# Optimization experiments

Measured on AMD Instinct MI355X. Metric: run time of the kernel, lower is better.

## Reference

```python
import jax, jax.numpy as jnp
import numpy as np

NEG_SLOPE = 0.2  # PyG GATConv default leaky_relu slope
BN_EPS = 1e-5


def gat_conv(x_src, x_dst, src, dst, w_src, w_dst, att_src, att_dst, bias):
    """Bipartite PyG GATConv, heads=H, concat=False (mean over heads), add_self_loops=True.
    x_src: [Ns, F], x_dst: [Nd, F]; src/dst: [E] int edge index; w_*: [F, H*C]; att_*: [H, C]; bias: [C].
    """
    H, C = att_src.shape
    n_dst = x_dst.shape[0]
    hs = (x_src @ w_src).reshape(-1, H, C)            # [Ns, H, C]
    hd = (x_dst @ w_dst).reshape(-1, H, C)            # [Nd, H, C]
    a_s = (hs * att_src[None]).sum(-1)                # [Ns, H]
    a_d = (hd * att_dst[None]).sum(-1)                # [Nd, H]
    # PyG adds self loops with num_nodes = min(Ns, Nd) for bipartite inputs
    n_loop = min(x_src.shape[0], n_dst)
    loop = jnp.arange(n_loop, dtype=src.dtype)
    src = jnp.concatenate([src, loop])
    dst = jnp.concatenate([dst, loop])
    e = jax.nn.leaky_relu(a_s[src] + a_d[dst], NEG_SLOPE)           # [E+L, H]
    m = jax.ops.segment_max(e, dst, num_segments=n_dst)             # [Nd, H]
    ex = jnp.exp(e - m[dst])
    den = jax.ops.segment_sum(ex, dst, num_segments=n_dst)
    alpha = ex / (den[dst] + 1e-16)                                 # neighborhood softmax
    msg = hs[src] * alpha[:, :, None]                               # [E+L, H, C]
    out = jax.ops.segment_sum(msg, dst, num_segments=n_dst)         # [Nd, H, C]
    return out.mean(axis=1) + bias


def _forward(user_ids, ingredient_ids, recipe_x, ing_src, ing_dst, ub_src, ub_dst,
             user_table, ing_table, W_rl, b_rl, bn_gamma, bn_beta,
             g1_ws, g1_wd, g1_as, g1_ad, g1_b,
             g2_ws, g2_wd, g2_as, g2_ad, g2_b):
    # nn.Embedding(max_norm=1.0): renorm looked-up rows to L2 norm <= 1
    u = user_table[user_ids]
    un = jnp.linalg.norm(u, axis=-1, keepdims=True)
    u = u * jnp.where(un > 1.0, 1.0 / (un + 1e-7), 1.0)
    # static ingredient embedding lookup
    ing = ing_table[ingredient_ids]
    # recipe linear + BatchNorm (training-mode batch stats; dropout off = eval)
    r = recipe_x @ W_rl + b_rl
    mu = r.mean(axis=0)
    var = ((r - mu) ** 2).mean(axis=0)
    r = bn_gamma * (r - mu) * jax.lax.rsqrt(var + BN_EPS) + bn_beta
    # ingredient -> recipe GAT, residual add
    r = r + gat_conv(ing, r, ing_src, ing_dst, g1_ws, g1_wd, g1_as, g1_ad, g1_b)
    # user -> recipe GAT
    r = gat_conv(u, r, ub_src, ub_dst, g2_ws, g2_wd, g2_as, g2_ad, g2_b)
    return r


def setup_inputs() -> dict:
    key = jax.random.key(0)
    ks = jax.random.split(key, 24)
    NU, NR, NI = 50000, 100000, 20000
    D_IN, H, C = 20, 2, 128
    E1, E2 = 400000, 800000
    s = 0.05
    f32 = jnp.float32
    inp = {
        "user_ids": jax.random.randint(ks[0], (NU,), 0, NU, dtype=jnp.int32),
        "ingredient_ids": jax.random.randint(ks[1], (NI,), 0, NI, dtype=jnp.int32),
        "recipe_x": jax.random.normal(ks[2], (NR, D_IN), f32),
        "ing_src": jax.random.randint(ks[3], (E1,), 0, NI, dtype=jnp.int32),
        "ing_dst": jax.random.randint(ks[4], (E1,), 0, NR, dtype=jnp.int32),
        "ub_src": jax.random.randint(ks[5], (E2,), 0, NU, dtype=jnp.int32),
        "ub_dst": jax.random.randint(ks[6], (E2,), 0, NR, dtype=jnp.int32),
        "user_table": jax.random.normal(ks[7], (NU, C), f32) * s,
        "ing_table": jax.random.normal(ks[8], (NI, C), f32) * s,
        "W_rl": jax.random.normal(ks[9], (D_IN, C), f32) * s,
        "b_rl": jnp.zeros((C,), f32),
        "bn_gamma": jnp.ones((C,), f32),
        "bn_beta": jnp.zeros((C,), f32),
        "g1_ws": jax.random.normal(ks[10], (C, H * C), f32) * s,
        "g1_wd": jax.random.normal(ks[11], (C, H * C), f32) * s,
        "g1_as": jax.random.normal(ks[12], (H, C), f32) * s,
        "g1_ad": jax.random.normal(ks[13], (H, C), f32) * s,
        "g1_b": jnp.zeros((C,), f32),
        "g2_ws": jax.random.normal(ks[14], (C, H * C), f32) * s,
        "g2_wd": jax.random.normal(ks[15], (C, H * C), f32) * s,
        "g2_as": jax.random.normal(ks[16], (H, C), f32) * s,
        "g2_ad": jax.random.normal(ks[17], (H, C), f32) * s,
        "g2_b": jnp.zeros((C,), f32),
    }
    return inp


def reference(user_ids, ingredient_ids, recipe_x, ing_src, ing_dst, ub_src, ub_dst,
              user_table, ing_table, W_rl, b_rl, bn_gamma, bn_beta,
              g1_ws, g1_wd, g1_as, g1_ad, g1_b,
              g2_ws, g2_wd, g2_as, g2_ad, g2_b):
    return _forward(user_ids, ingredient_ids, recipe_x, ing_src, ing_dst, ub_src, ub_dst,
                    user_table, ing_table, W_rl, b_rl, bn_gamma, bn_beta,
                    g1_ws, g1_wd, g1_as, g1_ad, g1_b,
                    g2_ws, g2_wd, g2_as, g2_ad, g2_b)
```

## Files before the change

### kernel.cpp

```cpp
#include <hip/hip_runtime.h>
#include <hip/hip_bf16.h>
#include <math.h>

#define DIN 20
#define C 128
#define HC 256
#define EB2 2048
#define MAXNB 400
#define CAP 8192
#define CAPSH 13

typedef unsigned short u16;
typedef unsigned int u32;
typedef unsigned long long u64;
typedef __bf16 bf16x8 __attribute__((ext_vector_type(8)));
typedef float f32x4 __attribute__((ext_vector_type(4)));

__device__ __forceinline__ float bfbits2f(unsigned int lo16) {
    return __uint_as_float(lo16 << 16);
}
__device__ __forceinline__ u16 f2bf_rne(float f) {
    unsigned int b = __float_as_uint(f);
    return (u16)((b + 0x7FFFu + ((b >> 16) & 1u)) >> 16);
}

__device__ __forceinline__ void scan512f(u32* cnt, u32* off, u32* wsum4) {
    int t = threadIdx.x;
    int l = t & 63, w = t >> 6;
    u32 a = cnt[2 * t], b = cnt[2 * t + 1];
    u32 s = a + b;
    u32 isc = s;
    #pragma unroll
    for (int o = 1; o < 64; o <<= 1) {
        u32 n = __shfl_up(isc, o);
        if (l >= o) isc += n;
    }
    if (l == 63) wsum4[w] = isc;
    __syncthreads();
    u32 pre = 0;
    if (w > 0) pre += wsum4[0];
    if (w > 1) pre += wsum4[1];
    if (w > 2) pre += wsum4[2];
    u32 excl = pre + isc - s;
    off[2 * t] = excl;
    off[2 * t + 1] = excl + a;
    __syncthreads();
}

__device__ __forceinline__ void edge_at(int i, const int* s1, const int* d1,
    const int* s2, const int* d2, int E1, int T1, int E2, int NR,
    int& s, int& key)
{
    if (i < T1) {
        if (i < E1) { s = s1[i]; key = d1[i]; }
        else        { s = i - E1; key = i - E1; }
    } else {
        int k = i - T1;
        if (k < E2) { s = s2[k]; key = NR + d2[k]; }
        else        { s = k - E2; key = NR + (k - E2); }
    }
}

__global__ __launch_bounds__(256) void k_init(const float* __restrict__ x, int NR,
    float* __restrict__ stats, int SB, int A2B,
    const int* __restrict__ src1, const int* __restrict__ dst1,
    const int* __restrict__ src2, const int* __restrict__ dst2,
    int E1, int L1, int E2, int L2, int NB,
    u32* __restrict__ bucketFill, u64* __restrict__ pairs,
    const float* __restrict__ g2_ws, u16* __restrict__ wsp,
    const float* __restrict__ g1_wd, const float* __restrict__ g1_ad,
    const float* __restrict__ g2_wd, const float* __restrict__ g2_ad,
    const float* __restrict__ g1_ws, const float* __restrict__ g1_as,
    const float* __restrict__ g2_as)
{
    __shared__ __align__(16) char sm[40528];
    int t = threadIdx.x;
    int bid = blockIdx.x;
    if (bid < SB) {
        float (*L)[DIN] = (float(*)[DIN])sm;
        int r = bid * 256 + t;
        if (r < NR) {
            const float4* xp = (const float4*)(x + (size_t)r * DIN);
            float4 v0 = xp[0], v1 = xp[1], v2 = xp[2], v3 = xp[3], v4 = xp[4];
            L[t][0] = v0.x; L[t][1] = v0.y; L[t][2] = v0.z; L[t][3] = v0.w;
            L[t][4] = v1.x; L[t][5] = v1.y; L[t][6] = v1.z; L[t][7] = v1.w;
            L[t][8] = v2.x; L[t][9] = v2.y; L[t][10] = v2.z; L[t][11] = v2.w;
            L[t][12] = v3.x; L[t][13] = v3.y; L[t][14] = v3.z; L[t][15] = v3.w;
            L[t][16] = v4.x; L[t][17] = v4.y; L[t][18] = v4.z; L[t][19] = v4.w;
        } else {
            #pragma unroll
            for (int k = 0; k < DIN; k++) L[t][k] = 0.f;
        }
        __syncthreads();
        if (t < 210) {
            int p = 0, q = t;
            while (q >= DIN - p) { q -= (DIN - p); p++; }
            q += p;
            float acc = 0.f;
            for (int rr = 0; rr < 256; rr++) acc += L[rr][p] * L[rr][q];
            atomicAdd(&stats[p * DIN + q], acc);
            if (p != q) atomicAdd(&stats[q * DIN + p], acc);
        } else if (t < 230) {
            int k = t - 210;
            float acc = 0.f;
            for (int rr = 0; rr < 256; rr++) acc += L[rr][k];
            atomicAdd(&stats[400 + k], acc);
        }
        return;
    }
    if (bid < SB + A2B) {
        u64* ldsE = (u64*)sm;
        u64* ldsS = ldsE + EB2;
        u32* cntA = (u32*)(ldsS + EB2);
        u32* cntB = cntA + 512;
        u32* offL = cntB + 512;
        u32* wsum4 = offL + 512;
        u32* gbase = wsum4 + 4;
        for (int i = t; i < 512; i += 256) { cntA[i] = 0; cntB[i] = 0; }
        __syncthreads();
        int T1 = E1 + L1, T = T1 + E2 + L2;
        int base = (bid - SB) * EB2;
        int nE = T - base; if (nE > EB2) nE = EB2;
        for (int j = t; j < nE; j += 256) {
            int s, key;
            edge_at(base + j, src1, dst1, src2, dst2, E1, T1, E2, NR, s, key);
            ldsE[j] = ((u64)(u32)key << 32) | (u32)s;
            atomicAdd(&cntA[key >> 9], 1u);
        }
        __syncthreads();
        scan512f(cntA, offL, wsum4);
        for (int b = t; b < NB; b += 256) {
            u32 c = cntA[b];
            gbase[b] = c ? (((u32)b << CAPSH) + atomicAdd(&bucketFill[b], c)) : 0u;
        }
        __syncthreads();
        for (int j = t; j < nE; j += 256) {
            u64 e = ldsE[j];
            u32 b = ((u32)(e >> 32)) >> 9;
            u32 r = atomicAdd(&cntB[b], 1u);
            ldsS[offL[b] + r] = e;
        }
        __syncthreads();
        for (int j = t; j < nE; j += 256) {
            u64 e = ldsS[j];
            u32 b = ((u32)(e >> 32)) >> 9;
            pairs[gbase[b] + ((u32)j - offL[b])] = e;
        }
        return;
    }
    if (bid < SB + A2B + 32) {
        int idx0 = ((bid - SB - A2B) * 256 + t) * 4;
        #pragma unroll
        for (int i = 0; i < 4; i++) {
            int flat = idx0 + i;
            int j = flat & 7;
            int lane = (flat >> 3) & 63;
            int kb = (flat >> 9) & 3;
            int nt = flat >> 11;
            int k = kb * 32 + (lane >> 4) * 8 + j;
            int n = nt * 16 + (lane & 15);
            wsp[flat] = f2bf_rne(g2_ws[k * HC + n]);
        }
        return;
    }
    int dr = bid - SB - A2B - 32;
    const float* wm = (dr == 0) ? g1_wd : (dr == 1) ? g2_wd : (dr == 2) ? g1_ws : g2_ws;
    const float* am = (dr == 0) ? g1_ad : (dr == 1) ? g2_ad : (dr == 2) ? g1_as : g2_as;
    int obase = (dr == 0) ? 676 : (dr == 1) ? 932 : (dr == 2) ? 1200 : 1456;
    {
        int k = t >> 1, h = t & 1;
        const float4* wp = (const float4*)(wm + k * HC + h * C);
        const float4* ap = (const float4*)(am + h * C);
        float acc = 0.f;
        #pragma unroll 4
        for (int q = 0; q < 32; q++) {
            float4 xv = wp[q], yv = ap[q];
            acc += xv.x * yv.x + xv.y * yv.y + xv.z * yv.z + xv.w * yv.w;
        }
        stats[obase + t] = acc;
    }
}

__global__ __launch_bounds__(256) void k_pre(float* __restrict__ stats,
    const float* __restrict__ W,
    const float* __restrict__ gamma, const float* __restrict__ beta,
    const float* __restrict__ g1_ws, const float* __restrict__ g1b, float invN)
{
    int t = threadIdx.x;
    __shared__ float Sm[420];
    __shared__ float Wm[DIN * C];
    __shared__ float vd1s[256];
    __shared__ float vd2s[256];
    __shared__ float sS[128];
    __shared__ float sSh[128];
    for (int i = t; i < 420; i += 256) Sm[i] = stats[i];
    for (int i = t; i < DIN * C; i += 256) Wm[i] = W[i];
    vd1s[t] = stats[676 + t];
    vd2s[t] = stats[932 + t];
    __syncthreads();
    if (t < C) {
        float w[DIN];
        #pragma unroll
        for (int k = 0; k < DIN; k++) w[k] = Wm[k * C + t];
        float mb = 0.f;
        #pragma unroll
        for (int k = 0; k < DIN; k++) mb += Sm[400 + k] * invN * w[k];
        float e2 = 0.f;
        for (int p = 0; p < DIN; p++) {
            float acc2 = 0.f;
            #pragma unroll
            for (int q = 0; q < DIN; q++) acc2 += Sm[p * DIN + q] * w[q];
            e2 += w[p] * acc2;
        }
        e2 *= invN;
        float var = e2 - mb * mb;
        float s = gamma[t] * rsqrtf(var + 1e-5f);
        float sh = beta[t] - s * mb;
        stats[420 + t] = s;
        stats[548 + t] = sh;
        sS[t] = s;
        sSh[t] = sh;
    }
    {
        int k = t >> 1, h = t & 1;
        const float4* ws1p = (const float4*)(g1_ws + k * HC + h * C);
        float t0 = 0.f, t1 = 0.f;
        #pragma unroll 4
        for (int q = 0; q < 32; q++) {
            float4 wv = ws1p[q];
            int c = q * 4;
            t0 += wv.x * vd2s[(c + 0) * 2 + 0] + wv.y * vd2s[(c + 1) * 2 + 0]
                + wv.z * vd2s[(c + 2) * 2 + 0] + wv.w * vd2s[(c + 3) * 2 + 0];
            t1 += wv.x * vd2s[(c + 0) * 2 + 1] + wv.y * vd2s[(c + 1) * 2 + 1]
                + wv.z * vd2s[(c + 2) * 2 + 1] + wv.w * vd2s[(c + 3) * 2 + 1];
        }
        stats[1712 + t * 2 + 0] = t0;
        stats[1712 + t * 2 + 1] = t1;
    }
    if (t < 2) {
        float cb = 0.f;
        for (int k = 0; k < C; k++) cb += g1b[k] * vd2s[k * 2 + t];
        stats[1188 + t] = cb;
    }
    __syncthreads();
    if (t < 80) {
        int k = t >> 2, h4 = t & 3, h = h4 & 1;
        const float* vs = (h4 < 2) ? vd1s : vd2s;
        float acc = 0.f;
        for (int c = 0; c < C; c++) acc += sS[c] * Wm[k * C + c] * vs[c * 2 + h];
        stats[2240 + t] = acc;
    } else if (t < 84) {
        int h4 = t - 80, h = h4 & 1;
        const float* vs = (h4 < 2) ? vd1s : vd2s;
        float acc = 0.f;
        for (int c = 0; c < C; c++) acc += sSh[c] * vs[c * 2 + h];
        stats[2320 + h4] = acc;
    }
}

__global__ __launch_bounds__(256) void k_fin(const u64* __restrict__ pairs,
    const u32* __restrict__ bucketFill, int n2, int NB, int R0B, int IB,
    int* __restrict__ off2, int* __restrict__ sorted,
    const float* __restrict__ x, int NR, const float* __restrict__ stats,
    float* __restrict__ a_d, float* __restrict__ advd,
    const float* __restrict__ ing_table, const int* __restrict__ ing_ids, int NI,
    float* __restrict__ a_si, float* __restrict__ psi,
    const float* __restrict__ user_table, const int* __restrict__ user_ids, int NU,
    const u16* __restrict__ wsp, u16* __restrict__ hs16, float* __restrict__ a_su)
{
    __shared__ __align__(16) char sm[30736];
    int t = threadIdx.x;
    int bid = blockIdx.x;
    if (bid < NB) {
        u32* cntA = (u32*)sm;
        u32* cntB = cntA + 512;
        u32* offL = cntB + 512;
        u32* wsum4 = offL + 512;
        u32* ldsS = wsum4 + 4;
        int b = bid;
        u32 beg = (u32)b << CAPSH;
        u32 fill = bucketFill[b];
        u32 end = beg + fill;
        int dstBase = b << 9;
        for (int i = t; i < 512; i += 256) { cntA[i] = 0; cntB[i] = 0; }
        __syncthreads();
        for (u32 j = beg + t; j < end; j += 256) {
            u32 key = (u32)(pairs[j] >> 32);
            atomicAdd(&cntA[key - dstBase], 1u);
        }
        __syncthreads();
        scan512f(cntA, offL, wsum4);
        for (int d = t; d < 512; d += 256) {
            int gk = dstBase + d;
            if (gk < n2) {
                int s0 = (int)(beg + offL[d]);
                off2[2 * gk] = s0;
                off2[2 * gk + 1] = s0 + (int)cntA[d];
            }
        }
        bool fast = fill <= 6144u;
        __syncthreads();
        for (u32 j = beg + t; j < end; j += 256) {
            u64 e = pairs[j];
            u32 d = (u32)(e >> 32) - dstBase;
            u32 r = atomicAdd(&cntB[d], 1u);
            u32 pos = offL[d] + r;
            if (fast) ldsS[pos] = (u32)e;
            else sorted[beg + pos] = (int)(u32)e;
        }
        __syncthreads();
        if (fast) {
            for (u32 j = t; j < fill; j += 256) sorted[beg + j] = (int)ldsS[j];
        }
        return;
    }
    if (bid < NB + R0B) {
        float* fv = (float*)sm;
        if (t < 84) fv[t] = stats[2240 + t];
        __syncthreads();
        int r = (bid - NB) * 256 + t;
        if (r < NR) {
            const float4* xp = (const float4*)(x + (size_t)r * DIN);
            float4 v0 = xp[0], v1 = xp[1], v2 = xp[2], v3 = xp[3], v4 = xp[4];
            float xv[20] = {v0.x, v0.y, v0.z, v0.w, v1.x, v1.y, v1.z, v1.w,
                            v2.x, v2.y, v2.z, v2.w, v3.x, v3.y, v3.z, v3.w,
                            v4.x, v4.y, v4.z, v4.w};
            float a0 = 0.f, a1 = 0.f, b0 = 0.f, b1 = 0.f;
            #pragma unroll
            for (int k = 0; k < DIN; k++) {
                float xvk = xv[k];
                a0 += xvk * fv[k * 4 + 0];
                a1 += xvk * fv[k * 4 + 1];
                b0 += xvk * fv[k * 4 + 2];
                b1 += xvk * fv[k * 4 + 3];
            }
            ((float2*)a_d)[r]  = make_float2(a0 + fv[80], a1 + fv[81]);
            ((float2*)advd)[r] = make_float2(b0 + fv[82], b1 + fv[83]);
        }
        return;
    }
    if (bid < NB + R0B + IB) {
        float* u1s = (float*)sm;
        float* Ts  = u1s + 256;
        u1s[t] = stats[1200 + t];
        Ts[t] = stats[1712 + t];
        Ts[256 + t] = stats[1968 + t];
        __syncthreads();
        int r = t >> 3, cg = t & 7;
        int row = (bid - NB - R0B) * 32 + r;
        float as0 = 0.f, as1 = 0.f, p00 = 0.f, p01 = 0.f, p10 = 0.f, p11 = 0.f;
        if (row < NI) {
            const float* xp = ing_table + (size_t)ing_ids[row] * C + cg * 16;
            #pragma unroll
            for (int q = 0; q < 4; q++) {
                float4 v = ((const float4*)xp)[q];
                float xvv[4] = {v.x, v.y, v.z, v.w};
                #pragma unroll
                for (int jj = 0; jj < 4; jj++) {
                    int k = cg * 16 + q * 4 + jj;
                    float xx = xvv[jj];
                    as0 += xx * u1s[k * 2 + 0];
                    as1 += xx * u1s[k * 2 + 1];
                    p00 += xx * Ts[k * 4 + 0];
                    p01 += xx * Ts[k * 4 + 1];
                    p10 += xx * Ts[k * 4 + 2];
                    p11 += xx * Ts[k * 4 + 3];
                }
            }
        }
        #pragma unroll
        for (int m = 1; m <= 4; m <<= 1) {
            as0 += __shfl_xor(as0, m); as1 += __shfl_xor(as1, m);
            p00 += __shfl_xor(p00, m); p01 += __shfl_xor(p01, m);
            p10 += __shfl_xor(p10, m); p11 += __shfl_xor(p11, m);
        }
        if (cg == 0 && row < NI) {
            ((float2*)a_si)[row] = make_float2(as0, as1);
            float4 pv; pv.x = p00; pv.y = p01; pv.z = p10; pv.w = p11;
            ((float4*)psi)[row] = pv;
        }
        return;
    }
    u16* A = (u16*)sm;
    float* u2s = (float*)(sm + 8704);
    u2s[t] = stats[1456 + t];
    int rowBase = (bid - NB - R0B - IB) * 32;
    int r = t >> 3, cg = t & 7;
    int row = rowBase + r;
    float xv[16];
    if (row < NU) {
        const float* xp = user_table + (size_t)user_ids[row] * C + cg * 16;
        #pragma unroll
        for (int q = 0; q < 4; q++) {
            float4 v = ((const float4*)xp)[q];
            xv[q * 4 + 0] = v.x; xv[q * 4 + 1] = v.y;
            xv[q * 4 + 2] = v.z; xv[q * 4 + 3] = v.w;
        }
    } else {
        #pragma unroll
        for (int q = 0; q < 16; q++) xv[q] = 0.f;
    }
    float ss = 0.f;
    #pragma unroll
    for (int q = 0; q < 16; q++) ss += xv[q] * xv[q];
    #pragma unroll
    for (int m = 1; m <= 4; m <<= 1) ss += __shfl_xor(ss, m);
    float nn = sqrtf(ss);
    float f = (nn > 1.f) ? 1.f / (nn + 1e-7f) : 1.f;
    float as0 = 0.f, as1 = 0.f;
    #pragma unroll
    for (int q = 0; q < 16; q++) {
        xv[q] *= f;
        int k = cg * 16 + q;
        as0 += xv[q] * u2s[k * 2 + 0];
        as1 += xv[q] * u2s[k * 2 + 1];
    }
    #pragma unroll
    for (int m = 1; m <= 4; m <<= 1) {
        as0 += __shfl_xor(as0, m); as1 += __shfl_xor(as1, m);
    }
    if (cg == 0 && row < NU) ((float2*)a_su)[row] = make_float2(as0, as1);
    {
        union { u16 h[16]; uint4 u4[2]; } pk;
        #pragma unroll
        for (int q = 0; q < 16; q++) pk.h[q] = f2bf_rne(xv[q]);
        uint4* dst = (uint4*)&A[r * 136 + cg * 16];
        dst[0] = pk.u4[0];
        dst[1] = pk.u4[1];
    }
    __syncthreads();
    int w = t >> 6, l = t & 63;
    int m15 = l & 15, q4 = l >> 4;
    bf16x8 afrag[2][4];
    #pragma unroll
    for (int mt = 0; mt < 2; mt++)
        #pragma unroll
        for (int kb = 0; kb < 4; kb++)
            afrag[mt][kb] = *(const bf16x8*)&A[(mt * 16 + m15) * 136 + kb * 32 + q4 * 8];
    f32x4 acc[2][4];
    #pragma unroll
    for (int mt = 0; mt < 2; mt++)
        #pragma unroll
        for (int i = 0; i < 4; i++) acc[mt][i] = (f32x4){0.f, 0.f, 0.f, 0.f};
    #pragma unroll
    for (int kb = 0; kb < 4; kb++) {
        #pragma unroll
        for (int i = 0; i < 4; i++) {
            int nt = w * 4 + i;
            bf16x8 bfrag = *(const bf16x8*)&wsp[((nt * 4 + kb) * 64 + l) * 8];
            acc[0][i] = __builtin_amdgcn_mfma_f32_16x16x32_bf16(afrag[0][kb], bfrag, acc[0][i], 0, 0, 0);
            acc[1][i] = __builtin_amdgcn_mfma_f32_16x16x32_bf16(afrag[1][kb], bfrag, acc[1][i], 0, 0, 0);
        }
    }
    #pragma unroll
    for (int mt = 0; mt < 2; mt++) {
        #pragma unroll
        for (int i = 0; i < 4; i++) {
            int col = (w * 4 + i) * 16 + m15;
            #pragma unroll
            for (int rr = 0; rr < 4; rr++) {
                int rw = rowBase + mt * 16 + q4 * 4 + rr;
                if (rw < NU) hs16[(size_t)rw * HC + col] = f2bf_rne(acc[mt][i][rr]);
            }
        }
    }
}

__global__ __launch_bounds__(256) void k_agg(const int* __restrict__ off2, const int* __restrict__ sorted,
    const float* __restrict__ a_si, const float* __restrict__ psi,
    const float* __restrict__ a_d1, const float* __restrict__ advd,
    const float* __restrict__ cb,
    const float* __restrict__ a_su, const u16* __restrict__ hs16,
    const float* __restrict__ bias, int NR, float* __restrict__ out)
{
    int wave = threadIdx.x >> 6, lane = threadIdx.x & 63;
    int d = blockIdx.x * 4 + wave;
    if (d >= NR) return;
    int beg = off2[2 * d], end = off2[2 * d + 1];
    float ad0 = a_d1[d * 2 + 0], ad1 = a_d1[d * 2 + 1];
    float w0s = 0.f, w1s = 0.f, a00 = 0.f, a01 = 0.f, a10 = 0.f, a11 = 0.f;
    for (int j = beg + lane; j < end; j += 64) {
        int s = sorted[j];
        float2 as = ((const float2*)a_si)[s];
        float e0 = as.x + ad0; e0 = (e0 >= 0.f) ? e0 : 0.2f * e0;
        float e1 = as.y + ad1; e1 = (e1 >= 0.f) ? e1 : 0.2f * e1;
        float x0 = __expf(e0), x1 = __expf(e1);
        float4 p = ((const float4*)psi)[s];
        w0s += x0; w1s += x1;
        a00 += x0 * p.x; a01 += x0 * p.y;
        a10 += x1 * p.z; a11 += x1 * p.w;
    }
    #pragma unroll
    for (int o = 1; o < 64; o <<= 1) {
        w0s += __shfl_xor(w0s, o); w1s += __shfl_xor(w1s, o);
        a00 += __shfl_xor(a00, o); a01 += __shfl_xor(a01, o);
        a10 += __shfl_xor(a10, o); a11 += __shfl_xor(a11, o);
    }
    float inv0g = 1.f / (w0s + 1e-16f), inv1g = 1.f / (w1s + 1e-16f);
    float r0 = advd[d * 2 + 0] + cb[0] + 0.5f * (a00 * inv0g + a10 * inv1g);
    float r1 = advd[d * 2 + 1] + cb[1] + 0.5f * (a01 * inv0g + a11 * inv1g);
    int i2 = NR + d;
    int beg2 = off2[2 * i2], end2 = off2[2 * i2 + 1];
    int head = lane >> 5;
    int q = lane & 31;
    u32 laneoff = (u32)(head * 256 + q * 8);
    int hsel = lane & 32;
    float adh = head ? r1 : r0;
    float wsum = 0.f;
    float acc0 = 0.f, acc1 = 0.f, acc2 = 0.f, acc3 = 0.f;
    const char* hbase = (const char*)hs16;

    for (int base = beg2; base < end2; base += 32) {
        int rem = end2 - base; if (rem > 32) rem = 32;
        int j = q; if (j >= rem) j = rem - 1;
        int sp = sorted[base + j];
        u32 boff = ((u32)sp) << 9;
        float asv = a_su[sp * 2 + head];
        float ee = asv + adh; ee = (ee >= 0.f) ? ee : 0.2f * ee;
        float wcomb = __expf(ee);
        int e = 0;
        for (; e + 4 <= rem; e += 4) {
            u32 b0 = __shfl(boff, e + 0), b1 = __shfl(boff, e + 1);
            u32 b2 = __shfl(boff, e + 2), b3 = __shfl(boff, e + 3);
            uint2 g0 = *(const uint2*)(hbase + (b0 + laneoff));
            uint2 g1 = *(const uint2*)(hbase + (b1 + laneoff));
            uint2 g2 = *(const uint2*)(hbase + (b2 + laneoff));
            uint2 g3 = *(const uint2*)(hbase + (b3 + laneoff));
            float W0 = __shfl(wcomb, hsel + e + 0);
            float W1 = __shfl(wcomb, hsel + e + 1);
            float W2 = __shfl(wcomb, hsel + e + 2);
            float W3 = __shfl(wcomb, hsel + e + 3);
            wsum += (W0 + W1) + (W2 + W3);
            acc0 += W0 * bfbits2f(g0.x & 0xFFFFu);
            acc1 += W0 * __uint_as_float(g0.x & 0xFFFF0000u);
            acc2 += W0 * bfbits2f(g0.y & 0xFFFFu);
            acc3 += W0 * __uint_as_float(g0.y & 0xFFFF0000u);
            acc0 += W1 * bfbits2f(g1.x & 0xFFFFu);
            acc1 += W1 * __uint_as_float(g1.x & 0xFFFF0000u);
            acc2 += W1 * bfbits2f(g1.y & 0xFFFFu);
            acc3 += W1 * __uint_as_float(g1.y & 0xFFFF0000u);
            acc0 += W2 * bfbits2f(g2.x & 0xFFFFu);
            acc1 += W2 * __uint_as_float(g2.x & 0xFFFF0000u);
            acc2 += W2 * bfbits2f(g2.y & 0xFFFFu);
            acc3 += W2 * __uint_as_float(g2.y & 0xFFFF0000u);
            acc0 += W3 * bfbits2f(g3.x & 0xFFFFu);
            acc1 += W3 * __uint_as_float(g3.x & 0xFFFF0000u);
            acc2 += W3 * bfbits2f(g3.y & 0xFFFFu);
            acc3 += W3 * __uint_as_float(g3.y & 0xFFFF0000u);
        }
        for (; e < rem; e++) {
            u32 b0 = __shfl(boff, e);
            float W = __shfl(wcomb, hsel + e);
            uint2 g = *(const uint2*)(hbase + (b0 + laneoff));
            wsum += W;
            acc0 += W * bfbits2f(g.x & 0xFFFFu);
            acc1 += W * __uint_as_float(g.x & 0xFFFF0000u);
            acc2 += W * bfbits2f(g.y & 0xFFFFu);
            acc3 += W * __uint_as_float(g.y & 0xFFFF0000u);
        }
    }
    float inv = 1.f / (wsum + 1e-16f);
    float v0 = acc0 * inv, v1 = acc1 * inv, v2 = acc2 * inv, v3 = acc3 * inv;
    v0 = 0.5f * (v0 + __shfl_xor(v0, 32));
    v1 = 0.5f * (v1 + __shfl_xor(v1, 32));
    v2 = 0.5f * (v2 + __shfl_xor(v2, 32));
    v3 = 0.5f * (v3 + __shfl_xor(v3, 32));
    if (lane < 32) {
        float4 bb = ((const float4*)bias)[q];
        float4 o;
        o.x = v0 + bb.x; o.y = v1 + bb.y; o.z = v2 + bb.z; o.w = v3 + bb.w;
        ((float4*)(out + (size_t)d * C))[q] = o;
    }
}

extern "C" void kernel_launch(void* const* d_in, const int* in_sizes, int n_in,
                              void* d_out, int out_size, void* d_ws, size_t ws_size,
                              hipStream_t stream) {
    const int*   user_ids       = (const int*)d_in[0];
    const int*   ingredient_ids = (const int*)d_in[1];
    const float* recipe_x       = (const float*)d_in[2];
    const int*   ing_src        = (const int*)d_in[3];
    const int*   ing_dst        = (const int*)d_in[4];
    const int*   ub_src         = (const int*)d_in[5];
    const int*   ub_dst         = (const int*)d_in[6];
    const float* user_table     = (const float*)d_in[7];
    const float* ing_table      = (const float*)d_in[8];
    const float* W_rl           = (const float*)d_in[9];
    const float* bn_gamma       = (const float*)d_in[11];
    const float* bn_beta        = (const float*)d_in[12];
    const float* g1_ws          = (const float*)d_in[13];
    const float* g1_wd          = (const float*)d_in[14];
    const float* g1_as          = (const float*)d_in[15];
    const float* g1_ad          = (const float*)d_in[16];
    const float* g1_b           = (const float*)d_in[17];
    const float* g2_ws          = (const float*)d_in[18];
    const float* g2_wd          = (const float*)d_in[19];
    const float* g2_as          = (const float*)d_in[20];
    const float* g2_ad          = (const float*)d_in[21];
    const float* g2_b           = (const float*)d_in[22];

    int NU = in_sizes[0];
    int NI = in_sizes[1];
    int NR = in_sizes[2] / DIN;
    int E1 = in_sizes[3];
    int E2 = in_sizes[5];
    int Nmax = (NI > NU) ? NI : NU;
    int L1 = (NI < NR) ? NI : NR;
    int L2 = (NU < NR) ? NU : NR;
    int Etot = E1 + L1 + E2 + L2;
    int n2 = 2 * NR;
    int NB = (n2 + 511) >> 9;

    char* w = (char*)d_ws;
    u16*   hs16  = (u16*)w;    w += (size_t)Nmax * HC * 2;
    float* a_si  = (float*)w;  w += (size_t)NI * 2 * 4;
    float* a_su  = (float*)w;  w += (size_t)NU * 2 * 4;
    float* psi   = (float*)w;  w += (size_t)NI * 4 * 4;
    float* a_d   = (float*)w;  w += (size_t)NR * 2 * 4;
    float* advd  = (float*)w;  w += (size_t)NR * 2 * 4;
    float* stats = (float*)w;  w += 2432 * 4;
    u32*   bucketFill = (u32*)w; w += MAXNB * 4;
    u16*   wsp   = (u16*)w;    w += 32768 * 2;
    int*   off2  = (int*)w;    w += (size_t)(2 * n2) * 4;
    int*   sorted= (int*)w;    w += (size_t)NB * CAP * 4;
    w = (char*)(((size_t)w + 15) & ~(size_t)15);
    u64*   pairs = (u64*)w;    w += (size_t)NB * CAP * 8;

    hipMemsetAsync(stats, 0, (2432 + MAXNB) * 4, stream);

    int SB  = (NR + 255) / 256;
    int A2B = (Etot + EB2 - 1) / EB2;
    k_init<<<SB + A2B + 32 + 4, 256, 0, stream>>>(recipe_x, NR, stats, SB, A2B,
                                              ing_src, ing_dst, ub_src, ub_dst,
                                              E1, L1, E2, L2, NB,
                                              bucketFill, pairs, g2_ws, wsp,
                                              g1_wd, g1_ad, g2_wd, g2_ad,
                                              g1_ws, g1_as, g2_as);
    k_pre<<<1, 256, 0, stream>>>(stats, W_rl, bn_gamma, bn_beta,
                                 g1_ws, g1_b, 1.0f / NR);
    int R0B = (NR + 255) / 256;
    int IB  = (NI + 31) / 32;
    int HB  = (NU + 31) / 32;
    k_fin<<<NB + R0B + IB + HB, 256, 0, stream>>>(pairs, bucketFill, n2, NB, R0B, IB,
                                                  off2, sorted,
                                                  recipe_x, NR, stats, a_d, advd,
                                                  ing_table, ingredient_ids, NI, a_si, psi,
                                                  user_table, user_ids, NU,
                                                  wsp, hs16, a_su);
    k_agg<<<(NR + 3) / 4, 256, 0, stream>>>(off2, sorted, a_si, psi, a_d, advd,
                                            stats + 1188, a_su, hs16, g2_b, NR,
                                            (float*)d_out);
}
```

Measured before the change: 300.7 us.

## Fold k_pre into init/fin kernels and pack bucket pairs into 32 bits

Removes the single-block k_pre launch. Its weight-projection work moves into one of k_init's tail blocks, and the BatchNorm stats and fold coefficients are recomputed redundantly in each recipe block of k_fin. Bucket pairs are packed as 9-bit local destination plus 17-bit source in a u32, halving the scatter traffic. This saves a serialized launch and memory bandwidth, at the cost of redundant per-block compute and a limit of 2^17 on source ids.

```diff
diff --git a/kernel.cpp b/kernel.cpp
--- a/kernel.cpp
+++ b/kernel.cpp
@@ -66,12 +66,12 @@
     const int* __restrict__ src1, const int* __restrict__ dst1,
     const int* __restrict__ src2, const int* __restrict__ dst2,
     int E1, int L1, int E2, int L2, int NB,
-    u32* __restrict__ bucketFill, u64* __restrict__ pairs,
+    u32* __restrict__ bucketFill, u32* __restrict__ pairs,
     const float* __restrict__ g2_ws, u16* __restrict__ wsp,
     const float* __restrict__ g1_wd, const float* __restrict__ g1_ad,
     const float* __restrict__ g2_wd, const float* __restrict__ g2_ad,
     const float* __restrict__ g1_ws, const float* __restrict__ g1_as,
-    const float* __restrict__ g2_as)
+    const float* __restrict__ g2_as, const float* __restrict__ g1b)
 {
     __shared__ __align__(16) char sm[40528];
     int t = threadIdx.x;
@@ -143,8 +143,9 @@
         __syncthreads();
         for (int j = t; j < nE; j += 256) {
             u64 e = ldsS[j];
-            u32 b = ((u32)(e >> 32)) >> 9;
-            pairs[gbase[b] + ((u32)j - offL[b])] = e;
+            u32 key = (u32)(e >> 32);
+            u32 b = key >> 9;
+            pairs[gbase[b] + ((u32)j - offL[b])] = ((key & 511u) << 17) | (u32)e;
         }
         return;
     }
@@ -167,11 +168,12 @@
     const float* wm = (dr == 0) ? g1_wd : (dr == 1) ? g2_wd : (dr == 2) ? g1_ws : g2_ws;
     const float* am = (dr == 0) ? g1_ad : (dr == 1) ? g2_ad : (dr == 2) ? g1_as : g2_as;
     int obase = (dr == 0) ? 676 : (dr == 1) ? 932 : (dr == 2) ? 1200 : 1456;
+    float* vd2l = (float*)sm;
+    float acc = 0.f;
     {
         int k = t >> 1, h = t & 1;
         const float4* wp = (const float4*)(wm + k * HC + h * C);
         const float4* ap = (const float4*)(am + h * C);
-        float acc = 0.f;
         #pragma unroll 4
         for (int q = 0; q < 32; q++) {
             float4 xv = wp[q], yv = ap[q];
@@ -179,49 +181,9 @@
         }
         stats[obase + t] = acc;
     }
-}
-
-__global__ __launch_bounds__(256) void k_pre(float* __restrict__ stats,
-    const float* __restrict__ W,
-    const float* __restrict__ gamma, const float* __restrict__ beta,
-    const float* __restrict__ g1_ws, const float* __restrict__ g1b, float invN)
-{
-    int t = threadIdx.x;
-    __shared__ float Sm[420];
-    __shared__ float Wm[DIN * C];
-    __shared__ float vd1s[256];
-    __shared__ float vd2s[256];
-    __shared__ float sS[128];
-    __shared__ float sSh[128];
-    for (int i = t; i < 420; i += 256) Sm[i] = stats[i];
-    for (int i = t; i < DIN * C; i += 256) Wm[i] = W[i];
-    vd1s[t] = stats[676 + t];
-    vd2s[t] = stats[932 + t];
-    __syncthreads();
-    if (t < C) {
-        float w[DIN];
-        #pragma unroll
-        for (int k = 0; k < DIN; k++) w[k] = Wm[k * C + t];
-        float mb = 0.f;
-        #pragma unroll
-        for (int k = 0; k < DIN; k++) mb += Sm[400 + k] * invN * w[k];
-        float e2 = 0.f;
-        for (int p = 0; p < DIN; p++) {
-            float acc2 = 0.f;
-            #pragma unroll
-            for (int q = 0; q < DIN; q++) acc2 += Sm[p * DIN + q] * w[q];
-            e2 += w[p] * acc2;
-        }
-        e2 *= invN;
-        float var = e2 - mb * mb;
-        float s = gamma[t] * rsqrtf(var + 1e-5f);
-        float sh = beta[t] - s * mb;
-        stats[420 + t] = s;
-        stats[548 + t] = sh;
-        sS[t] = s;
-        sSh[t] = sh;
-    }
-    {
+    if (dr == 1) {
+        vd2l[t] = acc;
+        __syncthreads();
         int k = t >> 1, h = t & 1;
         const float4* ws1p = (const float4*)(g1_ws + k * HC + h * C);
         float t0 = 0.f, t1 = 0.f;
@@ -229,39 +191,27 @@
         for (int q = 0; q < 32; q++) {
             float4 wv = ws1p[q];
             int c = q * 4;
-            t0 += wv.x * vd2s[(c + 0) * 2 + 0] + wv.y * vd2s[(c + 1) * 2 + 0]
-                + wv.z * vd2s[(c + 2) * 2 + 0] + wv.w * vd2s[(c + 3) * 2 + 0];
-            t1 += wv.x * vd2s[(c + 0) * 2 + 1] + wv.y * vd2s[(c + 1) * 2 + 1]
-                + wv.z * vd2s[(c + 2) * 2 + 1] + wv.w * vd2s[(c + 3) * 2 + 1];
+            t0 += wv.x * vd2l[(c + 0) * 2 + 0] + wv.y * vd2l[(c + 1) * 2 + 0]
+                + wv.z * vd2l[(c + 2) * 2 + 0] + wv.w * vd2l[(c + 3) * 2 + 0];
+            t1 += wv.x * vd2l[(c + 0) * 2 + 1] + wv.y * vd2l[(c + 1) * 2 + 1]
+                + wv.z * vd2l[(c + 2) * 2 + 1] + wv.w * vd2l[(c + 3) * 2 + 1];
         }
         stats[1712 + t * 2 + 0] = t0;
         stats[1712 + t * 2 + 1] = t1;
-    }
-    if (t < 2) {
-        float cb = 0.f;
-        for (int k = 0; k < C; k++) cb += g1b[k] * vd2s[k * 2 + t];
-        stats[1188 + t] = cb;
-    }
-    __syncthreads();
-    if (t < 80) {
-        int k = t >> 2, h4 = t & 3, h = h4 & 1;
-        const float* vs = (h4 < 2) ? vd1s : vd2s;
-        float acc = 0.f;
-        for (int c = 0; c < C; c++) acc += sS[c] * Wm[k * C + c] * vs[c * 2 + h];
-        stats[2240 + t] = acc;
-    } else if (t < 84) {
-        int h4 = t - 80, h = h4 & 1;
-        const float* vs = (h4 < 2) ? vd1s : vd2s;
-        float acc = 0.f;
-        for (int c = 0; c < C; c++) acc += sSh[c] * vs[c * 2 + h];
-        stats[2320 + h4] = acc;
-    }
-}
-
-__global__ __launch_bounds__(256) void k_fin(const u64* __restrict__ pairs,
+        if (t < 2) {
+            float cb = 0.f;
+            for (int k2 = 0; k2 < C; k2++) cb += g1b[k2] * vd2l[k2 * 2 + t];
+            stats[1188 + t] = cb;
+        }
+    }
+}
+
+__global__ __launch_bounds__(256) void k_fin(const u32* __restrict__ pairs,
     const u32* __restrict__ bucketFill, int n2, int NB, int R0B, int IB,
     int* __restrict__ off2, int* __restrict__ sorted,
     const float* __restrict__ x, int NR, const float* __restrict__ stats,
+    const float* __restrict__ W, const float* __restrict__ gamma,
+    const float* __restrict__ beta, float invN,
     float* __restrict__ a_d, float* __restrict__ advd,
     const float* __restrict__ ing_table, const int* __restrict__ ing_ids, int NI,
     float* __restrict__ a_si, float* __restrict__ psi,
@@ -285,8 +235,8 @@
         for (int i = t; i < 512; i += 256) { cntA[i] = 0; cntB[i] = 0; }
         __syncthreads();
         for (u32 j = beg + t; j < end; j += 256) {
-            u32 key = (u32)(pairs[j] >> 32);
-            atomicAdd(&cntA[key - dstBase], 1u);
+            u32 fine = pairs[j] >> 17;
+            atomicAdd(&cntA[fine], 1u);
         }
         __syncthreads();
         scan512f(cntA, offL, wsum4);
@@ -301,12 +251,13 @@
         bool fast = fill <= 6144u;
         __syncthreads();
         for (u32 j = beg + t; j < end; j += 256) {
-            u64 e = pairs[j];
-            u32 d = (u32)(e >> 32) - dstBase;
+            u32 p = pairs[j];
+            u32 d = p >> 17;
             u32 r = atomicAdd(&cntB[d], 1u);
             u32 pos = offL[d] + r;
-            if (fast) ldsS[pos] = (u32)e;
-            else sorted[beg + pos] = (int)(u32)e;
+            u32 src = p & 0x1FFFFu;
+            if (fast) ldsS[pos] = src;
+            else sorted[beg + pos] = (int)src;
         }
         __syncthreads();
         if (fast) {
@@ -315,8 +266,52 @@
         return;
     }
     if (bid < NB + R0B) {
-        float* fv = (float*)sm;
-        if (t < 84) fv[t] = stats[2240 + t];
+        float* Sm   = (float*)sm;
+        float* Wm   = Sm + 420;
+        float* vd1s = Wm + 2560;
+        float* vd2s = vd1s + 256;
+        float* sS   = vd2s + 256;
+        float* sSh  = sS + 128;
+        float* fv   = sSh + 128;
+        for (int i = t; i < 420; i += 256) Sm[i] = stats[i];
+        for (int i = t; i < DIN * C; i += 256) Wm[i] = W[i];
+        vd1s[t] = stats[676 + t];
+        vd2s[t] = stats[932 + t];
+        __syncthreads();
+        if (t < C) {
+            float w[DIN];
+            #pragma unroll
+            for (int k = 0; k < DIN; k++) w[k] = Wm[k * C + t];
+            float mb = 0.f;
+            #pragma unroll
+            for (int k = 0; k < DIN; k++) mb += Sm[400 + k] * invN * w[k];
+            float e2 = 0.f;
+            for (int p = 0; p < DIN; p++) {
+                float acc2 = 0.f;
+                #pragma unroll
+                for (int q = 0; q < DIN; q++) acc2 += Sm[p * DIN + q] * w[q];
+                e2 += w[p] * acc2;
+            }
+            e2 *= invN;
+            float var = e2 - mb * mb;
+            float s = gamma[t] * rsqrtf(var + 1e-5f);
+            sS[t] = s;
+            sSh[t] = beta[t] - s * mb;
+        }
+        __syncthreads();
+        if (t < 80) {
+            int k = t >> 2, h4 = t & 3, h = h4 & 1;
+            const float* vs = (h4 < 2) ? vd1s : vd2s;
+            float acc = 0.f;
+            for (int c = 0; c < C; c++) acc += sS[c] * Wm[k * C + c] * vs[c * 2 + h];
+            fv[t] = acc;
+        } else if (t < 84) {
+            int h4 = t - 80, h = h4 & 1;
+            const float* vs = (h4 < 2) ? vd1s : vd2s;
+            float acc = 0.f;
+            for (int c = 0; c < C; c++) acc += sSh[c] * vs[c * 2 + h];
+            fv[t] = acc;
+        }
         __syncthreads();
         int r = (bid - NB) * 256 + t;
         if (r < NR) {
@@ -623,8 +618,7 @@
     u16*   wsp   = (u16*)w;    w += 32768 * 2;
     int*   off2  = (int*)w;    w += (size_t)(2 * n2) * 4;
     int*   sorted= (int*)w;    w += (size_t)NB * CAP * 4;
-    w = (char*)(((size_t)w + 15) & ~(size_t)15);
-    u64*   pairs = (u64*)w;    w += (size_t)NB * CAP * 8;
+    u32*   pairs = (u32*)w;    w += (size_t)NB * CAP * 4;
 
     hipMemsetAsync(stats, 0, (2432 + MAXNB) * 4, stream);
 
@@ -635,15 +629,15 @@
                                               E1, L1, E2, L2, NB,
                                               bucketFill, pairs, g2_ws, wsp,
                                               g1_wd, g1_ad, g2_wd, g2_ad,
-                                              g1_ws, g1_as, g2_as);
-    k_pre<<<1, 256, 0, stream>>>(stats, W_rl, bn_gamma, bn_beta,
-                                 g1_ws, g1_b, 1.0f / NR);
+                                              g1_ws, g1_as, g2_as, g1_b);
     int R0B = (NR + 255) / 256;
     int IB  = (NI + 31) / 32;
     int HB  = (NU + 31) / 32;
     k_fin<<<NB + R0B + IB + HB, 256, 0, stream>>>(pairs, bucketFill, n2, NB, R0B, IB,
                                                   off2, sorted,
-                                                  recipe_x, NR, stats, a_d, advd,
+                                                  recipe_x, NR, stats,
+                                                  W_rl, bn_gamma, bn_beta, 1.0f / NR,
+                                                  a_d, advd,
                                                   ing_table, ingredient_ids, NI, a_si, psi,
                                                   user_table, user_ids, NU,
                                                   wsp, hs16, a_su);
```

Result: faster. 292.1 us (-2.9%).
